# Optimization experiments

Measured on AMD Instinct MI355X. Metric: run time of the kernel, lower is better.

Reference implementation:

```python
import jax, jax.numpy as jnp
import numpy as np

BETA = 1.0
EPS_MU = 1e-6
EPS_LOG = 1e-8
D_DIM = 2048
M_EVENTS = 16384
T_HORIZON = 100


def setup_inputs() -> dict:
    key = jax.random.key(0)
    k1, k2 = jax.random.split(key)
    # sorted event times in [0, T_HORIZON)
    t_events = jnp.sort(jax.random.uniform(k1, (M_EVENTS,), jnp.float32) * T_HORIZON)
    marks = jax.random.randint(k2, (M_EVENTS,), 0, D_DIM)  # int marks in {0..D-1}
    # learned params, init exactly as in torch module
    log_mu = jnp.full((D_DIM,), -3.0, jnp.float32)
    log_alpha = jnp.full((D_DIM, D_DIM), -4.0, jnp.float32)
    return {
        "t_events": t_events,
        "marks": marks,
        "T_max": T_HORIZON,
        "log_mu": log_mu,
        "log_alpha": log_alpha,
    }


def _loglik(t_events, log_mu, log_alpha, marks, T_max, beta=BETA):
    mu = jax.nn.softplus(log_mu) + EPS_MU          # [D]
    alpha = jax.nn.softplus(log_alpha)             # [D, D]
    D = mu.shape[0]
    # dt[0] = 0 so the first step leaves S (= zeros) untouched, matching the
    # torch loop which skips decay at n == 0.
    dt = jnp.concatenate([jnp.zeros((1,), t_events.dtype), jnp.diff(t_events)])  # [M]

    def step(S, xs):
        dt_n, d = xs
        S = jnp.exp(-beta * dt_n) * S              # exponential decay of state [D]
        lam_d = mu[d] + alpha[d] @ S               # intensity at event's mark
        S = S.at[d].add(1.0)                       # self-excitation bump
        return S, jnp.log(lam_d + EPS_LOG)

    _, log_lams = jax.lax.scan(step, jnp.zeros((D,), mu.dtype), (dt, marks))

    # compensator integral term
    T = jnp.asarray(T_max, t_events.dtype)
    one_minus_exp = 1.0 - jnp.exp(-beta * (T - t_events))          # [M]
    contrib = jax.ops.segment_sum(one_minus_exp, marks, num_segments=D)  # [D]
    integral = mu * T + alpha @ (contrib / beta)                   # [D]
    return log_lams.sum() - integral.sum()


def reference(t_events, marks, T_max, log_mu, log_alpha):
    return _loglik(t_events, log_mu, log_alpha, marks, T_max)
```

## Files before the change

kernel.cpp:

```cpp
#include <hip/hip_runtime.h>
#include <math.h>

#define D_DIM 2048
#define M_EV  16384
#define LCH   32
#define CCH   (M_EV / LCH)
#define SEG   32
#define NSEG  (CCH / SEG)
#define BETA  1.0f
#define CPB   8

__device__ __forceinline__ float softplus_f(float x){
  float e = __expf(-fabsf(x));
  return fmaxf(x, 0.0f) + __logf(1.0f + e);
}

__device__ __forceinline__ unsigned short f2bf(float f){
  unsigned b = __float_as_uint(f);
  return (unsigned short)((b + 0x7FFFu + ((b >> 16) & 1u)) >> 16);
}
__device__ __forceinline__ float bf2f(unsigned short u){
  return __uint_as_float(((unsigned)u) << 16);
}

__device__ __forceinline__ float decode_T(const void* p){
  unsigned bits = *(const unsigned*)p;
  float fv = __uint_as_float(bits);
  return (fv >= 1e-3f && fv <= 1e7f) ? fv : (float)(int)bits;
}

__device__ __forceinline__ float wave_red(float v){
  #pragma unroll
  for (int o = 32; o > 0; o >>= 1) v += __shfl_down(v, o);
  return v;
}

__global__ __launch_bounds__(256) void k_prep(
    const float* __restrict__ t, const int* __restrict__ m,
    const float* __restrict__ log_mu, const void* Tp,
    float* __restrict__ muw, float* __restrict__ SL,
    float* __restrict__ dchunk, float* __restrict__ cumdec,
    float* __restrict__ Aseg, float* __restrict__ Cpart,
    float* __restrict__ acc)
{
  __shared__ float Srow[8 * D_DIM];
  const int b = blockIdx.x, tid = threadIdx.x;
  if (b < 8){
    int j = b*256 + tid;
    float v = softplus_f(log_mu[j]) + 1e-6f;
    muw[j] = v;
    float s = wave_red(v);
    if ((tid & 63) == 0) Srow[tid >> 6] = s;
    __syncthreads();
    if (tid == 0) acc[8 + b] = (Srow[0]+Srow[1]) + (Srow[2]+Srow[3]);
  } else if (b < 72){
    float4* S4 = (float4*)Srow;
    const float4 z = make_float4(0.f,0.f,0.f,0.f);
    #pragma unroll
    for (int k = 0; k < 16; ++k) S4[k*256 + tid] = z;
    __syncthreads();
    const int i = (b-8)*256 + tid;
    const int c = i >> 5;
    if (c < CCH - 1){
      float tn = t[(c+1)*LCH];
      atomicAdd(&Srow[(tid >> 5)*D_DIM + m[i]], __expf(-BETA * (tn - t[i])));
    }
    __syncthreads();
    float4* G4 = (float4*)(SL + (size_t)(b-8) * (8*D_DIM));
    #pragma unroll
    for (int k = 0; k < 16; ++k) G4[k*256 + tid] = S4[k*256 + tid];
  } else if (b < 72 + CPB){
    float* Cl = Srow;
    float4* Cl4 = (float4*)Cl;
    const float4 z = make_float4(0.f,0.f,0.f,0.f);
    Cl4[tid*2] = z; Cl4[tid*2 + 1] = z;
    __syncthreads();
    const float T = decode_T(Tp);
    #pragma unroll
    for (int k = 0; k < 8; ++k){
      int i = (b-72)*2048 + k*256 + tid;
      atomicAdd(&Cl[m[i]], 1.0f - __expf(-BETA * (T - t[i])));
    }
    __syncthreads();
    float4* Cp4 = (float4*)(Cpart + (size_t)(b-72) * D_DIM);
    Cp4[tid*2]     = Cl4[tid*2];
    Cp4[tid*2 + 1] = Cl4[tid*2 + 1];
  } else {
    int c = (b-80)*256 + tid;
    float tc = t[c*LCH];
    dchunk[c] = (c < CCH-1) ? __expf(-BETA * (t[(c+1)*LCH] - tc)) : 1.0f;
    int s0c = (c >> 5) << 5;
    cumdec[c] = __expf(-BETA * (tc - t[s0c*LCH]));
    if (b == 80 && tid < NSEG){
      int s = tid;
      Aseg[s] = (s < NSEG-1)
        ? __expf(-BETA * (t[(s+1)*SEG*LCH] - t[s*SEG*LCH])) : 1.0f;
    }
    if (b == 81 && tid < 8) acc[tid] = 0.f;
  }
}

__global__ __launch_bounds__(256) void k_scan_alpha(
    float* __restrict__ SL, const float* __restrict__ dchunk,
    float* __restrict__ Carry, const float* __restrict__ la,
    const float* __restrict__ Cpart, unsigned short* __restrict__ sA,
    float* __restrict__ acc)
{
  const int b = blockIdx.x, tid = threadIdx.x;
  if (b < 128){
    const int seg = b >> 3, jb = b & 7;
    const int j = jb*256 + tid;
    const int c0 = seg * SEG;
    const size_t base = (size_t)c0 * D_DIM + j;
    float u = 0.f;
    float cur[4], nxt[4];
    #pragma unroll
    for (int q = 0; q < 4; ++q) cur[q] = SL[base + (size_t)q * D_DIM];
    for (int g = 0; g < SEG; g += 4){
      #pragma unroll
      for (int q = 0; q < 4; ++q)
        nxt[q] = (g+4 < SEG) ? SL[base + (size_t)(g+4+q) * D_DIM] : 0.f;
      #pragma unroll
      for (int q = 0; q < 4; ++q){
        int c = c0 + g + q;
        float l = cur[q];
        SL[(size_t)c * D_DIM + j] = u;
        u = fmaf(dchunk[c], u, l);
      }
      #pragma unroll
      for (int q = 0; q < 4; ++q) cur[q] = nxt[q];
    }
    Carry[(size_t)seg * D_DIM + j] = u;
    return;
  }
  const int nthreads = 512*256;
  int atid = (b-128)*256 + tid;
  const float4* Cp4 = (const float4*)Cpart;
  const int cq = atid & 511;
  float4 cb = make_float4(0.f,0.f,0.f,0.f);
  #pragma unroll
  for (int r = 0; r < CPB; ++r){
    float4 v = Cp4[r*512 + cq];
    cb.x += v.x; cb.y += v.y; cb.z += v.z; cb.w += v.w;
  }
  const float4* la4 = (const float4*)la;
  ushort4* sA4 = (ushort4*)sA;
  float p = 0.f;
  #pragma unroll
  for (int u = 0; u < 8; ++u){
    int i4 = atid + u * nthreads;
    float4 x = la4[i4];
    float4 sp;
    sp.x = softplus_f(x.x); sp.y = softplus_f(x.y);
    sp.z = softplus_f(x.z); sp.w = softplus_f(x.w);
    ushort4 h;
    h.x = f2bf(sp.x); h.y = f2bf(sp.y); h.z = f2bf(sp.z); h.w = f2bf(sp.w);
    sA4[i4] = h;
    p = fmaf(sp.x, cb.x, p);
    p = fmaf(sp.y, cb.y, p);
    p = fmaf(sp.z, cb.z, p);
    p = fmaf(sp.w, cb.w, p);
  }
  __shared__ float red[4];
  float w = wave_red(p);
  int lane = tid & 63, wid = tid >> 6;
  if (lane == 0) red[wid] = w;
  __syncthreads();
  if (tid == 0) atomicAdd(&acc[1], red[0]+red[1]+red[2]+red[3]);
}

__global__ __launch_bounds__(512) void k_events(
    const float* __restrict__ t, const int* __restrict__ m,
    const unsigned short* __restrict__ sA, const float* __restrict__ muw,
    const float* __restrict__ SL, const float* __restrict__ Carry,
    const float* __restrict__ Aseg, const float* __restrict__ cumdec,
    float* __restrict__ acc, const void* Tp, float* __restrict__ out){
  __shared__ float S0[D_DIM];
  __shared__ float tl[LCH];
  __shared__ int   ml[LCH];
  __shared__ float wred[8];
  const int tid = threadIdx.x;
  const int c = blockIdx.x;
  const int seg = c >> 5;
  const float cd = cumdec[c];

  {
    const float4 sv = *(const float4*)(SL + (size_t)c * D_DIM + tid*4);
    float4 e = {0.f, 0.f, 0.f, 0.f};
    float wgt = 1.f;
    for (int s = seg - 1; s >= 0; --s){
      const float4 cr = *(const float4*)(Carry + (size_t)s * D_DIM + tid*4);
      e.x = fmaf(cr.x, wgt, e.x); e.y = fmaf(cr.y, wgt, e.y);
      e.z = fmaf(cr.z, wgt, e.z); e.w = fmaf(cr.w, wgt, e.w);
      wgt *= Aseg[s];
    }
    float4 s;
    s.x = fmaf(e.x, cd, sv.x); s.y = fmaf(e.y, cd, sv.y);
    s.z = fmaf(e.z, cd, sv.z); s.w = fmaf(e.w, cd, sv.w);
    *(float4*)&S0[tid*4] = s;
  }
  if (tid < LCH){
    ml[tid] = m[c*LCH + tid];
    tl[tid] = t[c*LCH + tid];
  }
  __syncthreads();

  const int l = tid & 63, w = tid >> 6;
  const int l4 = l * 4;

  float4 s0[8];
  #pragma unroll
  for (int u = 0; u < 8; ++u) s0[u] = *(const float4*)&S0[u*256 + l4];

  const float t0 = tl[0];
  float lgw = 0.f;
  #pragma unroll
  for (int q = 0; q < 4; ++q){
    const int k = w*4 + q;
    const int d = ml[k];
    const unsigned short* row = sA + (size_t)d * D_DIM;
    float p = 0.f;
    #pragma unroll
    for (int u = 0; u < 8; ++u){
      ushort4 a = *(const ushort4*)(row + u*256 + l4);
      p = fmaf(bf2f(a.x), s0[u].x, p);
      p = fmaf(bf2f(a.y), s0[u].y, p);
      p = fmaf(bf2f(a.z), s0[u].z, p);
      p = fmaf(bf2f(a.w), s0[u].w, p);
    }
    const float tk = tl[k];
    float g = 0.f;
    if (l < k) g = bf2f(row[ml[l]]) * __expf(tl[l] - tk);
    p = fmaf(p, __expf(t0 - tk), g);
    float v = wave_red(p);
    if (l == 0) lgw += __logf(muw[d] + v + 1e-8f);
  }
  if (l == 0) wred[w] = lgw;
  __syncthreads();
  if (tid == 0){
    float lg = ((wred[0]+wred[1])+(wred[2]+wred[3]))
             + ((wred[4]+wred[5])+(wred[6]+wred[7]));
    atomicAdd(&acc[0], lg);
    __threadfence();
    unsigned old = atomicAdd((unsigned*)&acc[3], 1u);
    if (old == CCH - 1){
      float a0 = atomicAdd(&acc[0], 0.0f);
      float a1 = atomicAdd(&acc[1], 0.0f);
      float musum = 0.f;
      #pragma unroll
      for (int j = 8; j < 16; ++j) musum += atomicAdd(&acc[j], 0.0f);
      float T = decode_T(Tp);
      out[0] = a0 - (T * musum + a1 * (1.0f / BETA));
    }
  }
}

extern "C" void kernel_launch(void* const* d_in, const int* in_sizes, int n_in,
                              void* d_out, int out_size, void* d_ws, size_t ws_size,
                              hipStream_t stream) {
  const float* t_events  = (const float*)d_in[0];
  const int*   marks     = (const int*)  d_in[1];
  const void*  Tp        =               d_in[2];
  const float* log_mu    = (const float*)d_in[3];
  const float* log_alpha = (const float*)d_in[4];
  float* out = (float*)d_out;

  float* ws      = (float*)d_ws;
  float* SL      = ws;
  float* Carry   = SL + (size_t)CCH * D_DIM;
  float* muw     = Carry + (size_t)NSEG * D_DIM;
  float* dchunk  = muw + D_DIM;
  float* cumdec  = dchunk + CCH;
  float* Aseg    = cumdec + CCH;
  float* Cpart   = Aseg + NSEG;
  float* acc     = Cpart + (size_t)CPB * D_DIM;
  unsigned short* sA = (unsigned short*)(acc + 16);

  k_prep      <<<82, 256, 0, stream>>>(t_events, marks, log_mu, Tp, muw, SL,
                                       dchunk, cumdec, Aseg, Cpart, acc);
  k_scan_alpha<<<640, 256, 0, stream>>>(SL, dchunk, Carry, log_alpha, Cpart,
                                        sA, acc);
  k_events    <<<CCH, 512, 0, stream>>>(t_events, marks, sA, muw, SL, Carry,
                                        Aseg, cumdec, acc, Tp, out);
}
```

Measured before the change: 112.5 us.

## Fuse per-chunk decayed scatter into scan kernel via shared-memory tiles

The per-chunk decayed mark histograms are no longer built in k_prep and written to SL in global memory. The scan blocks now scatter the events of their segment into a shared-memory tile covering their 256-column slice, then run the chunk recurrence straight from shared memory. Chunk, segment and cumulative decay factors are recomputed inline instead of being stored in workspace arrays. This drops a full write and read of the SL matrix and shrinks k_prep, but each scan block now reads all 1024 events of its segment and filters them by column range, repeating those reads across 8 blocks.

```diff
diff --git a/kernel.cpp b/kernel.cpp
--- a/kernel.cpp
+++ b/kernel.cpp
@@ -7,6 +7,7 @@
 #define CCH   (M_EV / LCH)
 #define SEG   32
 #define NSEG  (CCH / SEG)
+#define EPSEG (SEG * LCH)
 #define BETA  1.0f
 #define CPB   8
 
@@ -38,39 +39,21 @@
 __global__ __launch_bounds__(256) void k_prep(
     const float* __restrict__ t, const int* __restrict__ m,
     const float* __restrict__ log_mu, const void* Tp,
-    float* __restrict__ muw, float* __restrict__ SL,
-    float* __restrict__ dchunk, float* __restrict__ cumdec,
-    float* __restrict__ Aseg, float* __restrict__ Cpart,
+    float* __restrict__ muw, float* __restrict__ Cpart,
     float* __restrict__ acc)
 {
-  __shared__ float Srow[8 * D_DIM];
+  __shared__ float Cl[D_DIM];
+  __shared__ float red[4];
   const int b = blockIdx.x, tid = threadIdx.x;
   if (b < 8){
     int j = b*256 + tid;
     float v = softplus_f(log_mu[j]) + 1e-6f;
     muw[j] = v;
     float s = wave_red(v);
-    if ((tid & 63) == 0) Srow[tid >> 6] = s;
-    __syncthreads();
-    if (tid == 0) acc[8 + b] = (Srow[0]+Srow[1]) + (Srow[2]+Srow[3]);
-  } else if (b < 72){
-    float4* S4 = (float4*)Srow;
-    const float4 z = make_float4(0.f,0.f,0.f,0.f);
-    #pragma unroll
-    for (int k = 0; k < 16; ++k) S4[k*256 + tid] = z;
-    __syncthreads();
-    const int i = (b-8)*256 + tid;
-    const int c = i >> 5;
-    if (c < CCH - 1){
-      float tn = t[(c+1)*LCH];
-      atomicAdd(&Srow[(tid >> 5)*D_DIM + m[i]], __expf(-BETA * (tn - t[i])));
-    }
-    __syncthreads();
-    float4* G4 = (float4*)(SL + (size_t)(b-8) * (8*D_DIM));
-    #pragma unroll
-    for (int k = 0; k < 16; ++k) G4[k*256 + tid] = S4[k*256 + tid];
-  } else if (b < 72 + CPB){
-    float* Cl = Srow;
+    if ((tid & 63) == 0) red[tid >> 6] = s;
+    __syncthreads();
+    if (tid == 0) acc[8 + b] = (red[0]+red[1]) + (red[2]+red[3]);
+  } else if (b < 8 + CPB){
     float4* Cl4 = (float4*)Cl;
     const float4 z = make_float4(0.f,0.f,0.f,0.f);
     Cl4[tid*2] = z; Cl4[tid*2 + 1] = z;
@@ -78,59 +61,68 @@
     const float T = decode_T(Tp);
     #pragma unroll
     for (int k = 0; k < 8; ++k){
-      int i = (b-72)*2048 + k*256 + tid;
+      int i = (b-8)*2048 + k*256 + tid;
       atomicAdd(&Cl[m[i]], 1.0f - __expf(-BETA * (T - t[i])));
     }
     __syncthreads();
-    float4* Cp4 = (float4*)(Cpart + (size_t)(b-72) * D_DIM);
+    float4* Cp4 = (float4*)(Cpart + (size_t)(b-8) * D_DIM);
     Cp4[tid*2]     = Cl4[tid*2];
     Cp4[tid*2 + 1] = Cl4[tid*2 + 1];
   } else {
-    int c = (b-80)*256 + tid;
-    float tc = t[c*LCH];
-    dchunk[c] = (c < CCH-1) ? __expf(-BETA * (t[(c+1)*LCH] - tc)) : 1.0f;
-    int s0c = (c >> 5) << 5;
-    cumdec[c] = __expf(-BETA * (tc - t[s0c*LCH]));
-    if (b == 80 && tid < NSEG){
-      int s = tid;
-      Aseg[s] = (s < NSEG-1)
-        ? __expf(-BETA * (t[(s+1)*SEG*LCH] - t[s*SEG*LCH])) : 1.0f;
-    }
-    if (b == 81 && tid < 8) acc[tid] = 0.f;
+    if (tid < 8) acc[tid] = 0.f;
   }
 }
 
 __global__ __launch_bounds__(256) void k_scan_alpha(
-    float* __restrict__ SL, const float* __restrict__ dchunk,
-    float* __restrict__ Carry, const float* __restrict__ la,
-    const float* __restrict__ Cpart, unsigned short* __restrict__ sA,
-    float* __restrict__ acc)
+    const float* __restrict__ t, const int* __restrict__ m,
+    float* __restrict__ SL, float* __restrict__ Carry,
+    const float* __restrict__ la, const float* __restrict__ Cpart,
+    unsigned short* __restrict__ sA, float* __restrict__ acc)
 {
+  __shared__ float Stile[SEG * 256];
+  __shared__ float tec[SEG];
+  __shared__ float dch[SEG];
   const int b = blockIdx.x, tid = threadIdx.x;
   if (b < 128){
     const int seg = b >> 3, jb = b & 7;
-    const int j = jb*256 + tid;
-    const int c0 = seg * SEG;
-    const size_t base = (size_t)c0 * D_DIM + j;
+    {
+      float4* S4 = (float4*)Stile;
+      const float4 z = make_float4(0.f,0.f,0.f,0.f);
+      #pragma unroll
+      for (int k = 0; k < 8; ++k) S4[k*256 + tid] = z;
+    }
+    if (tid < SEG){
+      int c = seg*SEG + tid;
+      if (c < CCH-1){
+        float te = t[(c+1)*LCH];
+        tec[tid] = te;
+        dch[tid] = __expf(t[c*LCH] - te);
+      } else {
+        tec[tid] = 0.f;
+        dch[tid] = 1.0f;
+      }
+    }
+    __syncthreads();
+    #pragma unroll
+    for (int e = 0; e < 4; ++e){
+      int il = e*256 + tid;
+      int i  = seg*EPSEG + il;
+      int cl = il >> 5;
+      int c  = seg*SEG + cl;
+      int mk = m[i] - jb*256;
+      if (c < CCH-1 && (unsigned)mk < 256u)
+        atomicAdd(&Stile[cl*256 + mk], __expf(t[i] - tec[cl]));
+    }
+    __syncthreads();
+    const int col = jb*256 + tid;
     float u = 0.f;
-    float cur[4], nxt[4];
-    #pragma unroll
-    for (int q = 0; q < 4; ++q) cur[q] = SL[base + (size_t)q * D_DIM];
-    for (int g = 0; g < SEG; g += 4){
-      #pragma unroll
-      for (int q = 0; q < 4; ++q)
-        nxt[q] = (g+4 < SEG) ? SL[base + (size_t)(g+4+q) * D_DIM] : 0.f;
-      #pragma unroll
-      for (int q = 0; q < 4; ++q){
-        int c = c0 + g + q;
-        float l = cur[q];
-        SL[(size_t)c * D_DIM + j] = u;
-        u = fmaf(dchunk[c], u, l);
-      }
-      #pragma unroll
-      for (int q = 0; q < 4; ++q) cur[q] = nxt[q];
-    }
-    Carry[(size_t)seg * D_DIM + j] = u;
+    #pragma unroll 4
+    for (int cl = 0; cl < SEG; ++cl){
+      int c = seg*SEG + cl;
+      SL[(size_t)c * D_DIM + col] = u;
+      u = fmaf(dch[cl], u, Stile[cl*256 + tid]);
+    }
+    Carry[(size_t)seg * D_DIM + col] = u;
     return;
   }
   const int nthreads = 512*256;
@@ -161,30 +153,38 @@
     p = fmaf(sp.z, cb.z, p);
     p = fmaf(sp.w, cb.w, p);
   }
-  __shared__ float red[4];
   float w = wave_red(p);
   int lane = tid & 63, wid = tid >> 6;
-  if (lane == 0) red[wid] = w;
-  __syncthreads();
-  if (tid == 0) atomicAdd(&acc[1], red[0]+red[1]+red[2]+red[3]);
+  if (lane == 0) Stile[wid] = w;
+  __syncthreads();
+  if (tid == 0) atomicAdd(&acc[1], Stile[0]+Stile[1]+Stile[2]+Stile[3]);
 }
 
 __global__ __launch_bounds__(512) void k_events(
     const float* __restrict__ t, const int* __restrict__ m,
     const unsigned short* __restrict__ sA, const float* __restrict__ muw,
     const float* __restrict__ SL, const float* __restrict__ Carry,
-    const float* __restrict__ Aseg, const float* __restrict__ cumdec,
     float* __restrict__ acc, const void* Tp, float* __restrict__ out){
   __shared__ float S0[D_DIM];
   __shared__ float tl[LCH];
   __shared__ int   ml[LCH];
   __shared__ float wred[8];
+  __shared__ float asg[16];
   const int tid = threadIdx.x;
   const int c = blockIdx.x;
   const int seg = c >> 5;
-  const float cd = cumdec[c];
+
+  if (tid < LCH){
+    ml[tid] = m[c*LCH + tid];
+    tl[tid] = t[c*LCH + tid];
+  } else if (tid >= 64 && tid < 64 + NSEG - 1){
+    int s = tid - 64;
+    asg[s] = __expf(t[s*EPSEG] - t[(s+1)*EPSEG]);
+  }
+  __syncthreads();
 
   {
+    const float cd = __expf(t[seg*EPSEG] - tl[0]);
     const float4 sv = *(const float4*)(SL + (size_t)c * D_DIM + tid*4);
     float4 e = {0.f, 0.f, 0.f, 0.f};
     float wgt = 1.f;
@@ -192,16 +192,12 @@
       const float4 cr = *(const float4*)(Carry + (size_t)s * D_DIM + tid*4);
       e.x = fmaf(cr.x, wgt, e.x); e.y = fmaf(cr.y, wgt, e.y);
       e.z = fmaf(cr.z, wgt, e.z); e.w = fmaf(cr.w, wgt, e.w);
-      wgt *= Aseg[s];
+      wgt *= asg[s];
     }
     float4 s;
     s.x = fmaf(e.x, cd, sv.x); s.y = fmaf(e.y, cd, sv.y);
     s.z = fmaf(e.z, cd, sv.z); s.w = fmaf(e.w, cd, sv.w);
     *(float4*)&S0[tid*4] = s;
-  }
-  if (tid < LCH){
-    ml[tid] = m[c*LCH + tid];
-    tl[tid] = t[c*LCH + tid];
   }
   __syncthreads();
 
@@ -269,17 +265,14 @@
   float* SL      = ws;
   float* Carry   = SL + (size_t)CCH * D_DIM;
   float* muw     = Carry + (size_t)NSEG * D_DIM;
-  float* dchunk  = muw + D_DIM;
-  float* cumdec  = dchunk + CCH;
-  float* Aseg    = cumdec + CCH;
-  float* Cpart   = Aseg + NSEG;
+  float* Cpart   = muw + D_DIM;
   float* acc     = Cpart + (size_t)CPB * D_DIM;
   unsigned short* sA = (unsigned short*)(acc + 16);
 
-  k_prep      <<<82, 256, 0, stream>>>(t_events, marks, log_mu, Tp, muw, SL,
-                                       dchunk, cumdec, Aseg, Cpart, acc);
-  k_scan_alpha<<<640, 256, 0, stream>>>(SL, dchunk, Carry, log_alpha, Cpart,
-                                        sA, acc);
+  k_prep      <<<17, 256, 0, stream>>>(t_events, marks, log_mu, Tp,
+                                       muw, Cpart, acc);
+  k_scan_alpha<<<640, 256, 0, stream>>>(t_events, marks, SL, Carry,
+                                        log_alpha, Cpart, sA, acc);
   k_events    <<<CCH, 512, 0, stream>>>(t_events, marks, sA, muw, SL, Carry,
-                                        Aseg, cumdec, acc, Tp, out);
-}
+                                        acc, Tp, out);
+}
```

Result: no change. 113.4 us (+0.8%).
